# Optimization experiments

Hardware: AMD Instinct MI355X
Metric: run time of the kernel (lower is better)

## Reference

```python
import jax, jax.numpy as jnp
import numpy as np

B, S, TAGSET = 64, 512, 62
T = TAGSET + 2  # + START (index T-2) and END (index T-1)


def setup_inputs() -> dict:
    key = jax.random.key(0)
    k1, k2, k3, k4 = jax.random.split(key, 4)
    feats = jax.random.normal(k1, (B, S, T), dtype=jnp.float32)
    # transitions param (torch init is zeros; small random for a non-degenerate baseline)
    transitions = 0.01 * jax.random.normal(k2, (T, T), dtype=jnp.float32)
    # variable-length contiguous-prefix mask (CRF assumes mask[:, 0] == 1)
    lengths = jax.random.randint(k3, (B,), S // 2, S + 1)
    mask = (jnp.arange(S)[None, :] < lengths[:, None]).astype(jnp.int32)
    tags = jax.random.randint(k4, (B, S), 0, TAGSET).astype(jnp.int32)
    return {"feats": feats, "transitions": transitions, "mask": mask, "tags": tags}


def _nll(feats, transitions, mask, tags):
    b, s, t = feats.shape
    maskb = mask.astype(bool)
    feats_t = jnp.transpose(feats, (1, 0, 2))  # [S, B, T]
    mask_t = jnp.transpose(maskb, (1, 0))       # [S, B]

    # ---- partition function (calculate_PZ) ----
    start = t - 2
    init_part = feats_t[0] + transitions[start][None, :]  # [B, T]

    def step(part, inp):
        f_t, m_t = inp  # f_t: [B, T] emissions, m_t: [B]
        # scores[b, i, j] = part[b, i] + transitions[i, j] + f_t[b, j]
        cur = jax.nn.logsumexp(
            part[:, :, None] + transitions[None, :, :] + f_t[:, None, :], axis=1
        )  # [B, T]
        part = jnp.where(m_t[:, None], cur, part)
        return part, None

    part, _ = jax.lax.scan(step, init_part, (feats_t[1:], mask_t[1:]))
    final = jax.nn.logsumexp(part[:, :, None] + transitions[None, :, :], axis=1)
    forward_score = final[:, t - 1].sum()  # transition into END

    # ---- gold score (score_sentence) ----
    tags = tags.astype(jnp.int32)
    prev = jnp.concatenate(
        [jnp.full((b, 1), start, dtype=jnp.int32), tags[:, :-1]], axis=1
    )  # [B, S] previous tag (START at t=0)
    emit = jnp.take_along_axis(feats, tags[..., None].astype(jnp.int32), axis=2)[..., 0]
    trans = transitions[prev, tags]  # [B, S]
    tg_energy = jnp.where(maskb, emit + trans, 0.0).sum()
    lengths = mask.astype(jnp.int32).sum(axis=1)  # [B]
    end_ids = jnp.take_along_axis(tags, (lengths - 1)[:, None], axis=1)[:, 0]
    end_energy = transitions[end_ids, t - 1].sum()
    gold_score = tg_energy + end_energy

    return forward_score - gold_score


def reference(feats, transitions, mask, tags):
    return _nll(feats, transitions, mask, tags)
```

## Files before the change

### kernel.cpp

```cpp
#include <hip/hip_runtime.h>


#define SS 512
#define TT 64
#define CC 16
#define KCH 32
#define START_TAG 62
#define END_TAG 63
#define LOG2E_F 1.44269504088896340736f
#define LN2_F 0.69314718055994530942f

#define WS_ECOL_OFF 8388608
#define MSTR 72

typedef float v4f __attribute__((ext_vector_type(4)));
typedef _Float16 h4 __attribute__((ext_vector_type(4)));
typedef __fp16 c2 __attribute__((ext_vector_type(2)));
union H4u { h4 v; struct { c2 lo, hi; } p; };

__device__ __forceinline__ void estep(const h4 (&A)[4][4], h4 (&B)[4],
                                      const float* __restrict__ emrow,
                                      int q, int& esum, int& esc) {
    v4f z = {0.f, 0.f, 0.f, 0.f};
    v4f D[4];
#pragma unroll
    for (int mt = 0; mt < 4; ++mt) {
        v4f a = __builtin_amdgcn_mfma_f32_16x16x16f16(A[mt][0], B[0], z, 0, 0, 0);
        a = __builtin_amdgcn_mfma_f32_16x16x16f16(A[mt][1], B[1], a, 0, 0, 0);
        v4f b = __builtin_amdgcn_mfma_f32_16x16x16f16(A[mt][2], B[2], z, 0, 0, 0);
        b = __builtin_amdgcn_mfma_f32_16x16x16f16(A[mt][3], B[3], b, 0, 0, 0);
        D[mt] = a + b;
    }
    esum += esc;
    float scf = __uint_as_float((unsigned)(127 - esc) << 23);
    v4f qs[4];
#pragma unroll
    for (int mt = 0; mt < 4; ++mt) {
        v4f em = *(const v4f*)(emrow + 16 * mt + 4 * q);
        qs[mt] = D[mt] * (em * scf);
    }
#pragma unroll
    for (int mt = 0; mt < 4; ++mt) {
        H4u u;
        u.p.lo = __builtin_amdgcn_cvt_pkrtz(qs[mt].x, qs[mt].y);
        u.p.hi = __builtin_amdgcn_cvt_pkrtz(qs[mt].z, qs[mt].w);
        B[mt] = u.v;
    }
    unsigned u0 = (unsigned)__builtin_amdgcn_readfirstlane((int)__float_as_uint(qs[0].x));
    esc = (int)((u0 >> 23) & 255u) - 127;
}

__global__ __launch_bounds__(256, 4)
void crf_chunks(const float* __restrict__ feats, const float* __restrict__ trans,
                const int* __restrict__ mask, unsigned short* __restrict__ Pg,
                int* __restrict__ Eg, float* __restrict__ out) {
    __shared__ __align__(16) float emS[KCH][TT];
    __shared__ __align__(16) _Float16 mldB[TT * MSTR];
    __shared__ __align__(16) _Float16 mldD[TT * MSTR];
    __shared__ int ebuf[12];

    const int blk = blockIdx.x;
    const int chain = blk >> 4, c = blk & 15;
    const int tid = threadIdx.x;
    const int w = tid >> 6, l = tid & 63;
    const int n16 = l & 15, q = l >> 4;
    const int ncol = 16 * w + n16;

    if (blk == 0 && tid == 0) out[0] = 0.f;

    h4 A[4][4];
#pragma unroll
    for (int mt = 0; mt < 4; ++mt)
#pragma unroll
        for (int ks = 0; ks < 4; ++ks) {
            h4 a;
#pragma unroll
            for (int e = 0; e < 4; ++e)
                a[e] = (_Float16)__builtin_amdgcn_exp2f(
                    trans[(16 * ks + 4 * q + e) * TT + 16 * mt + n16] * LOG2E_F);
            A[mt][ks] = a;
        }

    const int* mp = mask + chain * SS;
    int msum = 0;
#pragma unroll
    for (int k = 0; k < 8; ++k) msum += mp[k * 64 + l];
#pragma unroll
    for (int s_ = 1; s_ < 64; s_ <<= 1) msum += __shfl_xor(msum, s_, 64);
    const int L = msum;

    const int t0a = 1 + KCH * c;
    const int base = (L - 1) - KCH * c;
    int nA = base < 0 ? 0 : (base > 8 ? 8 : base);
    int nB = base - 8 < 0 ? 0 : (base - 8 > 8 ? 8 : base - 8);
    int nC = base - 16 < 0 ? 0 : (base - 16 > 8 ? 8 : base - 16);
    int nD = base - 24 < 0 ? 0 : (base - 24 > 8 ? 8 : base - 24);

    const float* fbase = feats + (size_t)chain * SS * TT;
#pragma unroll
    for (int k = 0; k < 2; ++k) {
        int idx = tid + 256 * k;
        int row = idx >> 4;
        int seg = idx & 15;
        int t = t0a + row;
        t = t < SS ? t : SS - 1;
        v4f v = *(const v4f*)(fbase + (size_t)t * TT + 4 * seg);
        v4f e;
        e.x = __builtin_amdgcn_exp2f(v.x * LOG2E_F);
        e.y = __builtin_amdgcn_exp2f(v.y * LOG2E_F);
        e.z = __builtin_amdgcn_exp2f(v.z * LOG2E_F);
        e.w = __builtin_amdgcn_exp2f(v.w * LOG2E_F);
        *(v4f*)(&emS[row][4 * seg]) = e;
    }

    h4 Ba[4], Bb[4], Bc[4], Bd[4];
#pragma unroll
    for (int ks = 0; ks < 4; ++ks) {
        h4 b;
#pragma unroll
        for (int jj = 0; jj < 4; ++jj)
            b[jj] = (_Float16)((16 * ks + 4 * q + jj == ncol) ? 1.f : 0.f);
        Ba[ks] = b; Bb[ks] = b; Bc[ks] = b; Bd[ks] = b;
    }
    __syncthreads();

    int esA = 0, escA = 0, esB = 0, escB = 0;
    int esC = 0, escC = 0, esD = 0, escD = 0;

    if (nD == 8) {
        for (int r = 0; r < 4; ++r) {
            const int s0 = 2 * r, s1 = s0 + 1;
            estep(A, Ba, &emS[s0][0],      q, esA, escA);
            estep(A, Bb, &emS[8 + s0][0],  q, esB, escB);
            estep(A, Bc, &emS[16 + s0][0], q, esC, escC);
            estep(A, Bd, &emS[24 + s0][0], q, esD, escD);
            estep(A, Ba, &emS[s1][0],      q, esA, escA);
            estep(A, Bb, &emS[8 + s1][0],  q, esB, escB);
            estep(A, Bc, &emS[16 + s1][0], q, esC, escC);
            estep(A, Bd, &emS[24 + s1][0], q, esD, escD);
        }
    } else {
        for (int r = 0; r < 4; ++r) {
            const int s0 = 2 * r, s1 = s0 + 1;
            if (s0 < nA) estep(A, Ba, &emS[s0][0],      q, esA, escA);
            if (s0 < nB) estep(A, Bb, &emS[8 + s0][0],  q, esB, escB);
            if (s0 < nC) estep(A, Bc, &emS[16 + s0][0], q, esC, escC);
            if (s0 < nD) estep(A, Bd, &emS[24 + s0][0], q, esD, escD);
            if (s1 < nA) estep(A, Ba, &emS[s1][0],      q, esA, escA);
            if (s1 < nB) estep(A, Bb, &emS[8 + s1][0],  q, esB, escB);
            if (s1 < nC) estep(A, Bc, &emS[16 + s1][0], q, esC, escC);
            if (s1 < nD) estep(A, Bd, &emS[24 + s1][0], q, esD, escD);
        }
    }

    if (l == 0) { ebuf[w] = esB; ebuf[4 + w] = esD; }
    __syncthreads();
    const int eBmax = max(max(ebuf[0], ebuf[1]), max(ebuf[2], ebuf[3]));
    const int eDmax = max(max(ebuf[4], ebuf[5]), max(ebuf[6], ebuf[7]));
    {
        _Float16 sB = (_Float16)ldexpf(1.f, esB - eBmax);
        _Float16 sD = (_Float16)ldexpf(1.f, esD - eDmax);
        h4 s4B = {sB, sB, sB, sB}, s4D = {sD, sD, sD, sD};
#pragma unroll
        for (int ks = 0; ks < 4; ++ks) {
            h4 vb = Bb[ks] * s4B;
            h4 vd = Bd[ks] * s4D;
#pragma unroll
            for (int jj = 0; jj < 4; ++jj) {
                mldB[(16 * ks + 4 * q + jj) * MSTR + ncol] = vb[jj];
                mldD[(16 * ks + 4 * q + jj) * MSTR + ncol] = vd[jj];
            }
        }
    }
    __syncthreads();
    h4 AHb[4][4], AHd[4][4];
#pragma unroll
    for (int mt = 0; mt < 4; ++mt)
#pragma unroll
        for (int ks = 0; ks < 4; ++ks) {
            AHb[mt][ks] = *(const h4*)(mldB + (16 * mt + n16) * MSTR + 16 * ks + 4 * q);
            AHd[mt][ks] = *(const h4*)(mldD + (16 * mt + n16) * MSTR + 16 * ks + 4 * q);
        }
    v4f z = {0.f, 0.f, 0.f, 0.f};
    v4f P1[4], P2[4];
#pragma unroll
    for (int mt = 0; mt < 4; ++mt) {
        v4f a = __builtin_amdgcn_mfma_f32_16x16x16f16(AHb[mt][0], Ba[0], z, 0, 0, 0);
        a = __builtin_amdgcn_mfma_f32_16x16x16f16(AHb[mt][1], Ba[1], a, 0, 0, 0);
        v4f b = __builtin_amdgcn_mfma_f32_16x16x16f16(AHb[mt][2], Ba[2], z, 0, 0, 0);
        b = __builtin_amdgcn_mfma_f32_16x16x16f16(AHb[mt][3], Ba[3], b, 0, 0, 0);
        P1[mt] = a + b;
        v4f a2 = __builtin_amdgcn_mfma_f32_16x16x16f16(AHd[mt][0], Bc[0], z, 0, 0, 0);
        a2 = __builtin_amdgcn_mfma_f32_16x16x16f16(AHd[mt][1], Bc[1], a2, 0, 0, 0);
        v4f b2 = __builtin_amdgcn_mfma_f32_16x16x16f16(AHd[mt][2], Bc[2], z, 0, 0, 0);
        b2 = __builtin_amdgcn_mfma_f32_16x16x16f16(AHd[mt][3], Bc[3], b2, 0, 0, 0);
        P2[mt] = a2 + b2;
    }
    float m1 = 0.f, m2 = 0.f;
#pragma unroll
    for (int mt = 0; mt < 4; ++mt) {
        m1 = fmaxf(m1, fmaxf(fmaxf(P1[mt].x, P1[mt].y), fmaxf(P1[mt].z, P1[mt].w)));
        m2 = fmaxf(m2, fmaxf(fmaxf(P2[mt].x, P2[mt].y), fmaxf(P2[mt].z, P2[mt].w)));
    }
#pragma unroll
    for (int m = 1; m < 64; m <<= 1) {
        m1 = fmaxf(m1, __shfl_xor(m1, m, 64));
        m2 = fmaxf(m2, __shfl_xor(m2, m, 64));
    }
    unsigned u1 = (unsigned)__builtin_amdgcn_readfirstlane((int)__float_as_uint(m1));
    unsigned u2 = (unsigned)__builtin_amdgcn_readfirstlane((int)__float_as_uint(m2));
    const int e1c = u1 ? (int)((u1 >> 23) & 255u) - 127 : 0;
    const int e2c = u2 ? (int)((u2 >> 23) & 255u) - 127 : 0;
    const int e1 = esA + eBmax + e1c;
    const int e2 = esC + eDmax + e2c;
    h4 P1h[4], P2h[4];
    {
        float s1f = __uint_as_float((unsigned)(127 - e1c) << 23);
        float s2f = __uint_as_float((unsigned)(127 - e2c) << 23);
#pragma unroll
        for (int mt = 0; mt < 4; ++mt) {
            v4f q1 = P1[mt] * s1f;
            v4f q2 = P2[mt] * s2f;
            H4u ua, ub;
            ua.p.lo = __builtin_amdgcn_cvt_pkrtz(q1.x, q1.y);
            ua.p.hi = __builtin_amdgcn_cvt_pkrtz(q1.z, q1.w);
            ub.p.lo = __builtin_amdgcn_cvt_pkrtz(q2.x, q2.y);
            ub.p.hi = __builtin_amdgcn_cvt_pkrtz(q2.z, q2.w);
            P1h[mt] = ua.v;
            P2h[mt] = ub.v;
        }
    }

    if (l == 0) ebuf[8 + w] = e2;
    __syncthreads();
    const int e2max = max(max(ebuf[8], ebuf[9]), max(ebuf[10], ebuf[11]));
    {
        _Float16 s2 = (_Float16)ldexpf(1.f, e2 - e2max);
        h4 s4 = {s2, s2, s2, s2};
#pragma unroll
        for (int mt = 0; mt < 4; ++mt) {
            h4 v = P2h[mt] * s4;
#pragma unroll
            for (int jj = 0; jj < 4; ++jj)
                mldB[(16 * mt + 4 * q + jj) * MSTR + ncol] = v[jj];
        }
    }
    __syncthreads();
    h4 AHp[4][4];
#pragma unroll
    for (int mt = 0; mt < 4; ++mt)
#pragma unroll
        for (int ks = 0; ks < 4; ++ks)
            AHp[mt][ks] = *(const h4*)(mldB + (16 * mt + n16) * MSTR + 16 * ks + 4 * q);
    h4 Rf[4];
#pragma unroll
    for (int mt = 0; mt < 4; ++mt) {
        v4f a = __builtin_amdgcn_mfma_f32_16x16x16f16(AHp[mt][0], P1h[0], z, 0, 0, 0);
        a = __builtin_amdgcn_mfma_f32_16x16x16f16(AHp[mt][1], P1h[1], a, 0, 0, 0);
        v4f b = __builtin_amdgcn_mfma_f32_16x16x16f16(AHp[mt][2], P1h[2], z, 0, 0, 0);
        b = __builtin_amdgcn_mfma_f32_16x16x16f16(AHp[mt][3], P1h[3], b, 0, 0, 0);
        v4f d = a + b;
        H4u u;
        u.p.lo = __builtin_amdgcn_cvt_pkrtz(d.x, d.y);
        u.p.hi = __builtin_amdgcn_cvt_pkrtz(d.z, d.w);
        Rf[mt] = u.v;
    }
    __syncthreads();
#pragma unroll
    for (int mt = 0; mt < 4; ++mt)
#pragma unroll
        for (int jj = 0; jj < 4; ++jj)
            mldD[(16 * mt + 4 * q + jj) * MSTR + ncol] = Rf[mt][jj];
    __syncthreads();
    {
        const size_t base_ = ((size_t)chain * CC + c) * 4096;
        int r = tid >> 2, cb = tid & 3;
        const uint4* src = (const uint4*)(mldD + r * MSTR + cb * 16);
        uint4* dst = (uint4*)(Pg + base_ + r * TT + cb * 16);
        dst[0] = src[0];
        dst[1] = src[1];
    }
    if (q == 0) Eg[(chain * CC + c) * TT + ncol] = e1 + e2max;
}

__device__ __forceinline__ int wimax64(int v) {
#pragma unroll
    for (int m = 1; m < 64; m <<= 1) v = max(v, __shfl_xor(v, m, 64));
    return v;
}
__device__ __forceinline__ float wfmax64(float v) {
#pragma unroll
    for (int m = 1; m < 64; m <<= 1) v = fmaxf(v, __shfl_xor(v, m, 64));
    return v;
}
__device__ __forceinline__ float wfsum64(float v) {
#pragma unroll
    for (int m = 1; m < 64; m <<= 1) v += __shfl_xor(v, m, 64);
    return v;
}
__device__ __forceinline__ int fexp(float m) {
    unsigned u = (unsigned)__builtin_amdgcn_readfirstlane((int)__float_as_uint(m));
    return u ? (int)((u >> 23) & 255u) - 127 : 0;
}
__device__ __forceinline__ void loadrow(uint4 (&h)[8], const unsigned short* __restrict__ PgC,
                                        int c, int l) {
    const uint4* rp = (const uint4*)((const _Float16*)PgC + (size_t)c * 4096) + l * 8;
#pragma unroll
    for (int i = 0; i < 8; ++i) h[i] = rp[i];
}
__device__ __forceinline__ void mvstep(const uint4 (&hv)[8], int e, float* __restrict__ xws,
                                       int l, float& x, int& exX) {
    int emax = wimax64(e);
    float xt = ldexpf(x, e - emax);
    xws[l] = xt;
    float acc = 0.f;
#pragma unroll
    for (int i = 0; i < 8; ++i) {
        union { uint4 u; _Float16 hh[8]; } pv;
        pv.u = hv[i];
        v4f xa = *(const v4f*)(xws + 8 * i);
        v4f xb = *(const v4f*)(xws + 8 * i + 4);
        acc = __builtin_fmaf((float)pv.hh[0], xa.x, acc);
        acc = __builtin_fmaf((float)pv.hh[1], xa.y, acc);
        acc = __builtin_fmaf((float)pv.hh[2], xa.z, acc);
        acc = __builtin_fmaf((float)pv.hh[3], xa.w, acc);
        acc = __builtin_fmaf((float)pv.hh[4], xb.x, acc);
        acc = __builtin_fmaf((float)pv.hh[5], xb.y, acc);
        acc = __builtin_fmaf((float)pv.hh[6], xb.z, acc);
        acc = __builtin_fmaf((float)pv.hh[7], xb.w, acc);
    }
    float am = wfmax64(acc);
    int e0 = fexp(am);
    x = ldexpf(acc, -e0);
    exX += e0 + emax;
}

__global__ __launch_bounds__(256, 1)
void crf_combine(const float* __restrict__ feats, const float* __restrict__ trans,
                 const int* __restrict__ mask, const int* __restrict__ tags,
                 const unsigned short* __restrict__ Pg, const int* __restrict__ Eg,
                 float* __restrict__ out) {
    __shared__ __align__(16) float xsh[4][TT];
    __shared__ float gred[4];

    const int chain = blockIdx.x;
    const int tid = threadIdx.x;
    const int w = tid >> 6, l = tid & 63;
    const unsigned short* PgC = Pg + (size_t)chain * CC * 4096;
    const int* EgC = Eg + chain * CC * TT;
    const float* fbase = feats + (size_t)chain * SS * TT;

    int msum = 0;
#pragma unroll
    for (int k = 0; k < 8; ++k) msum += mask[chain * SS + 64 * k + l];
#pragma unroll
    for (int m = 1; m < 64; m <<= 1) msum += __shfl_xor(msum, m, 64);
    const int L = msum;

    float g = 0.f;
#pragma unroll
    for (int rep = 0; rep < 2; ++rep) {
        int t = tid + rep * 256;
        if (t < L) {
            int cur = tags[chain * SS + t];
            int prev = t ? tags[chain * SS + t - 1] : START_TAG;
            g += fbase[(size_t)t * TT + cur] + trans[prev * TT + cur];
        }
    }
    g = wfsum64(g);
    if (l == 0) gred[w] = g;

    float pl = fbase[l] + trans[START_TAG * TT + l];
    float M0 = wfmax64(pl);
    float x = __builtin_amdgcn_exp2f((pl - M0) * LOG2E_F);
    int exX = 0;

    uint4 hA[8], hB[8];
    int eA, eB;
    loadrow(hA, PgC, 0, l);
    eA = EgC[0 * TT + l];
#pragma unroll
    for (int c = 0; c < CC; c += 2) {
        loadrow(hB, PgC, c + 1, l);
        eB = EgC[(c + 1) * TT + l];
        mvstep(hA, eA, &xsh[w][0], l, x, exX);
        if (c + 2 < CC) {
            loadrow(hA, PgC, c + 2, l);
            eA = EgC[(c + 2) * TT + l];
        }
        mvstep(hB, eB, &xsh[w][0], l, x, exX);
    }

    float val = x * expf(trans[l * TT + END_TAG]);
    val = wfsum64(val);
    float fwd = logf(val) + (float)exX * LN2_F + M0;

    __syncthreads();
    if (tid == 0) {
        float gold = gred[0] + gred[1] + gred[2] + gred[3] +
                     trans[tags[chain * SS + L - 1] * TT + END_TAG];
        atomicAdd(out, fwd - gold);
    }
}

extern "C" void kernel_launch(void* const* d_in, const int* in_sizes, int n_in,
                              void* d_out, int out_size, void* d_ws, size_t ws_size,
                              hipStream_t stream) {
    const float* feats = (const float*)d_in[0];
    const float* trans = (const float*)d_in[1];
    const int*   mask  = (const int*)d_in[2];
    const int*   tags  = (const int*)d_in[3];
    float* out = (float*)d_out;
    unsigned short* Pg = (unsigned short*)d_ws;
    int*       Eg = (int*)((char*)d_ws + WS_ECOL_OFF);

    crf_chunks<<<dim3(64 * CC), dim3(256), 0, stream>>>(feats, trans, mask, Pg, Eg, out);
    crf_combine<<<dim3(64), dim3(256), 0, stream>>>(feats, trans, mask, tags, Pg, Eg, out);
}
```

Baseline: 114.5 us.

## Store emissions as fp16 in LDS, scale in fp16, and early-exit empty chunks

Converts exponentiated emissions to fp16 before storing them in LDS. The per-step emission multiply now happens in packed fp16 after the pkrtz conversion, and the renormalisation exponent is read from the fp16 result, with an extra bias of 2 to leave headroom. Chunks that lie entirely beyond the sequence length now write an identity matrix and zero exponents, then return early, so they skip the transition-exp setup and the MFMA chain. This shortens each step of the serial recurrence and removes idle work, at the cost of fp16 overflow/underflow risk in the emission product.

```diff
diff --git a/kernel.cpp b/kernel.cpp
--- a/kernel.cpp
+++ b/kernel.cpp
@@ -19,7 +19,7 @@
 union H4u { h4 v; struct { c2 lo, hi; } p; };
 
 __device__ __forceinline__ void estep(const h4 (&A)[4][4], h4 (&B)[4],
-                                      const float* __restrict__ emrow,
+                                      const _Float16* __restrict__ emrow,
                                       int q, int& esum, int& esc) {
     v4f z = {0.f, 0.f, 0.f, 0.f};
     v4f D[4];
@@ -31,30 +31,28 @@
         b = __builtin_amdgcn_mfma_f32_16x16x16f16(A[mt][3], B[3], b, 0, 0, 0);
         D[mt] = a + b;
     }
-    esum += esc;
-    float scf = __uint_as_float((unsigned)(127 - esc) << 23);
-    v4f qs[4];
+    esum += esc + 2;
+    float scf = __uint_as_float((unsigned)(125 - esc) << 23);
 #pragma unroll
     for (int mt = 0; mt < 4; ++mt) {
-        v4f em = *(const v4f*)(emrow + 16 * mt + 4 * q);
-        qs[mt] = D[mt] * (em * scf);
-    }
-#pragma unroll
-    for (int mt = 0; mt < 4; ++mt) {
+        v4f t = D[mt] * scf;
         H4u u;
-        u.p.lo = __builtin_amdgcn_cvt_pkrtz(qs[mt].x, qs[mt].y);
-        u.p.hi = __builtin_amdgcn_cvt_pkrtz(qs[mt].z, qs[mt].w);
-        B[mt] = u.v;
-    }
-    unsigned u0 = (unsigned)__builtin_amdgcn_readfirstlane((int)__float_as_uint(qs[0].x));
-    esc = (int)((u0 >> 23) & 255u) - 127;
+        u.p.lo = __builtin_amdgcn_cvt_pkrtz(t.x, t.y);
+        u.p.hi = __builtin_amdgcn_cvt_pkrtz(t.z, t.w);
+        h4 em4 = *(const h4*)(emrow + 16 * mt + 4 * q);
+        B[mt] = u.v * em4;
+    }
+    _Float16 b0 = B[0][0];
+    unsigned short us = __builtin_bit_cast(unsigned short, b0);
+    unsigned ui = (unsigned)__builtin_amdgcn_readfirstlane((int)us);
+    esc = (int)((ui >> 10) & 31u) - 15;
 }
 
 __global__ __launch_bounds__(256, 4)
 void crf_chunks(const float* __restrict__ feats, const float* __restrict__ trans,
                 const int* __restrict__ mask, unsigned short* __restrict__ Pg,
                 int* __restrict__ Eg, float* __restrict__ out) {
-    __shared__ __align__(16) float emS[KCH][TT];
+    __shared__ __align__(16) _Float16 emS[KCH][TT];
     __shared__ __align__(16) _Float16 mldB[TT * MSTR];
     __shared__ __align__(16) _Float16 mldD[TT * MSTR];
     __shared__ int ebuf[12];
@@ -68,6 +66,28 @@
 
     if (blk == 0 && tid == 0) out[0] = 0.f;
 
+    const int* mp = mask + chain * SS;
+    int msum = 0;
+#pragma unroll
+    for (int k = 0; k < 8; ++k) msum += mp[k * 64 + l];
+#pragma unroll
+    for (int s_ = 1; s_ < 64; s_ <<= 1) msum += __shfl_xor(msum, s_, 64);
+    const int L = msum;
+
+    const int basei = (L - 1) - KCH * c;
+    if (basei <= 0) {
+        int r = tid >> 2, cb = tid & 3;
+        unsigned short buf[16];
+#pragma unroll
+        for (int j = 0; j < 16; ++j)
+            buf[j] = (16 * cb + j == r) ? (unsigned short)0x3C00 : (unsigned short)0;
+        uint4* dst = (uint4*)(Pg + ((size_t)chain * CC + c) * 4096 + r * TT + cb * 16);
+        dst[0] = *(const uint4*)(buf);
+        dst[1] = *(const uint4*)(buf + 8);
+        if (q == 0) Eg[(chain * CC + c) * TT + ncol] = 0;
+        return;
+    }
+
     h4 A[4][4];
 #pragma unroll
     for (int mt = 0; mt < 4; ++mt)
@@ -81,20 +101,11 @@
             A[mt][ks] = a;
         }
 
-    const int* mp = mask + chain * SS;
-    int msum = 0;
-#pragma unroll
-    for (int k = 0; k < 8; ++k) msum += mp[k * 64 + l];
-#pragma unroll
-    for (int s_ = 1; s_ < 64; s_ <<= 1) msum += __shfl_xor(msum, s_, 64);
-    const int L = msum;
-
     const int t0a = 1 + KCH * c;
-    const int base = (L - 1) - KCH * c;
-    int nA = base < 0 ? 0 : (base > 8 ? 8 : base);
-    int nB = base - 8 < 0 ? 0 : (base - 8 > 8 ? 8 : base - 8);
-    int nC = base - 16 < 0 ? 0 : (base - 16 > 8 ? 8 : base - 16);
-    int nD = base - 24 < 0 ? 0 : (base - 24 > 8 ? 8 : base - 24);
+    int nA = basei < 0 ? 0 : (basei > 8 ? 8 : basei);
+    int nB = basei - 8 < 0 ? 0 : (basei - 8 > 8 ? 8 : basei - 8);
+    int nC = basei - 16 < 0 ? 0 : (basei - 16 > 8 ? 8 : basei - 16);
+    int nD = basei - 24 < 0 ? 0 : (basei - 24 > 8 ? 8 : basei - 24);
 
     const float* fbase = feats + (size_t)chain * SS * TT;
 #pragma unroll
@@ -105,12 +116,12 @@
         int t = t0a + row;
         t = t < SS ? t : SS - 1;
         v4f v = *(const v4f*)(fbase + (size_t)t * TT + 4 * seg);
-        v4f e;
-        e.x = __builtin_amdgcn_exp2f(v.x * LOG2E_F);
-        e.y = __builtin_amdgcn_exp2f(v.y * LOG2E_F);
-        e.z = __builtin_amdgcn_exp2f(v.z * LOG2E_F);
-        e.w = __builtin_amdgcn_exp2f(v.w * LOG2E_F);
-        *(v4f*)(&emS[row][4 * seg]) = e;
+        H4u u;
+        u.p.lo = __builtin_amdgcn_cvt_pkrtz(__builtin_amdgcn_exp2f(v.x * LOG2E_F),
+                                            __builtin_amdgcn_exp2f(v.y * LOG2E_F));
+        u.p.hi = __builtin_amdgcn_cvt_pkrtz(__builtin_amdgcn_exp2f(v.z * LOG2E_F),
+                                            __builtin_amdgcn_exp2f(v.w * LOG2E_F));
+        *(h4*)(&emS[row][4 * seg]) = u.v;
     }
 
     h4 Ba[4], Bb[4], Bc[4], Bd[4];
```

Measured after the change: 114.9 us. No clear change (+0.4%).
